# Kernel optimization log

Measured on AMD Instinct MI355X. Metric: run time of the kernel, lower is better.

Reference implementation:

```python
import jax, jax.numpy as jnp
import numpy as np

N = 50000    # nodes
E = 800000   # edges (avg degree 16)
B = 256      # graphs in the batch (static for segment ops)
H = 128      # feature / hidden width (channels[-2])
NL = 4       # LSTM layers in Set2Set
PS = 4       # Set2Set processing steps
OUT = 2      # channels[-1]


def _bn(h, g, b):
    # BatchNorm1d with batch statistics (training-mode math, biased variance)
    m = h.mean(0)
    v = jnp.mean((h - m) ** 2, 0)
    return (h - m) * jax.lax.rsqrt(v + 1e-5) * g + b


def _gin(x, src, dst, W1, b1, ga1, be1, W2, b2, ga2, be2):
    # GINConv, eps=0: out = MLP(x + sum_{j->i} x_j)
    agg = jax.ops.segment_sum(x[src], dst, num_segments=x.shape[0])
    h = x + agg
    h = jax.nn.relu(_bn(h @ W1.T + b1, ga1, be1))
    h = jax.nn.relu(_bn(h @ W2.T + b2, ga2, be2))
    return h


def _set2set(x, batch, Wih0, Whh0, b0, WihR, WhhR, bR):
    hs = [jnp.zeros((B, H), x.dtype)] * NL
    cs = [jnp.zeros((B, H), x.dtype)] * NL
    q_star = jnp.zeros((B, 2 * H), x.dtype)
    for _ in range(PS):
        inp = q_star
        nhs, ncs = [], []
        for l in range(NL):  # stacked LSTM cells, seq-len 1 per step
            Wih = Wih0 if l == 0 else WihR[l - 1]
            Whh = Whh0 if l == 0 else WhhR[l - 1]
            bb = b0 if l == 0 else bR[l - 1]
            gates = inp @ Wih.T + hs[l] @ Whh.T + bb
            i, f, g, o = jnp.split(gates, 4, axis=-1)  # torch gate order i,f,g,o
            c = jax.nn.sigmoid(f) * cs[l] + jax.nn.sigmoid(i) * jnp.tanh(g)
            h = jax.nn.sigmoid(o) * jnp.tanh(c)
            nhs.append(h); ncs.append(c)
            inp = h
        hs, cs = nhs, ncs
        q = inp  # (B, H) top-layer hidden
        # per-graph segment softmax attention
        e = jnp.sum(x * q[batch], -1)                        # (N,)
        m = jax.ops.segment_max(e, batch, num_segments=B)
        ee = jnp.exp(e - m[batch])
        s = jax.ops.segment_sum(ee, batch, num_segments=B)
        a = ee / s[batch]
        r = jax.ops.segment_sum(a[:, None] * x, batch, num_segments=B)  # (B, H)
        q_star = jnp.concatenate([q, r], -1)
    return q_star


def setup_inputs() -> dict:
    key = jax.random.key(0)
    ks = jax.random.split(key, 16)

    def w(k, shape):
        return jax.random.normal(k, shape, jnp.float32) * 0.05

    d = {}
    d["x"] = jax.random.normal(ks[0], (N, H), jnp.float32)
    d["edge_index"] = jax.random.randint(ks[1], (2, E), 0, N, dtype=jnp.int32)
    d["batch"] = jnp.sort(jax.random.randint(ks[2], (N,), 0, B, dtype=jnp.int32))
    for i, g in enumerate(("g0", "g1")):
        kk = jax.random.split(ks[3 + i], 2)
        d[g + "_W1"] = w(kk[0], (H, H)); d[g + "_b1"] = jnp.zeros((H,), jnp.float32)
        d[g + "_gamma1"] = jnp.ones((H,), jnp.float32); d[g + "_beta1"] = jnp.zeros((H,), jnp.float32)
        d[g + "_W2"] = w(kk[1], (H, H)); d[g + "_b2"] = jnp.zeros((H,), jnp.float32)
        d[g + "_gamma2"] = jnp.ones((H,), jnp.float32); d[g + "_beta2"] = jnp.zeros((H,), jnp.float32)
    d["Wih0"] = w(ks[6], (4 * H, 2 * H))
    d["Whh0"] = w(ks[7], (4 * H, H))
    d["b0"] = jnp.zeros((4 * H,), jnp.float32)
    d["WihR"] = w(ks[8], (NL - 1, 4 * H, H))
    d["WhhR"] = w(ks[9], (NL - 1, 4 * H, H))
    d["bR"] = jnp.zeros((NL - 1, 4 * H), jnp.float32)
    d["lin_W"] = w(ks[10], (OUT, 2 * H))
    d["lin_b"] = jnp.zeros((OUT,), jnp.float32)
    return d


def reference(x, edge_index, batch,
              g0_W1, g0_b1, g0_gamma1, g0_beta1, g0_W2, g0_b2, g0_gamma2, g0_beta2,
              g1_W1, g1_b1, g1_gamma1, g1_beta1, g1_W2, g1_b2, g1_gamma2, g1_beta2,
              Wih0, Whh0, b0, WihR, WhhR, bR, lin_W, lin_b):
    src, dst = edge_index[0], edge_index[1]
    x = _gin(x, src, dst, g0_W1, g0_b1, g0_gamma1, g0_beta1, g0_W2, g0_b2, g0_gamma2, g0_beta2)
    x = _gin(x, src, dst, g1_W1, g1_b1, g1_gamma1, g1_beta1, g1_W2, g1_b2, g1_gamma2, g1_beta2)
    q = _set2set(x, batch, Wih0, Whh0, b0, WihR, WhhR, bR)
    # F.dropout(p=0.1) is identity in eval mode
    return q @ lin_W.T + lin_b
```

## Files before the change

kernel.cpp:

```cpp
#include <hip/hip_runtime.h>
#include <math.h>

#define NN 50000
#define EE 800000
#define BBG 256
#define HHC 128
#define SEG_CAP 448
#define ESC 512
#define NBIN 196
#define NBLK 196

typedef _Float16 half8 __attribute__((ext_vector_type(8)));
typedef _Float16 half4 __attribute__((ext_vector_type(4)));
typedef _Float16 half2v __attribute__((ext_vector_type(2)));
typedef float f32x4 __attribute__((ext_vector_type(4)));

#if defined(__has_builtin)
#if __has_builtin(__builtin_amdgcn_fdot2)
#define USE_FDOT2 1
#endif
#endif

__device__ __forceinline__ float fdot2f(half2v a, half2v b, float c) {
#ifdef USE_FDOT2
  return __builtin_amdgcn_fdot2(a, b, c, false);
#else
  return fmaf((float)a[0], (float)b[0], fmaf((float)a[1], (float)b[1], c));
#endif
}

__device__ __forceinline__ float fsigm(float x) {
  return __builtin_amdgcn_rcpf(1.f + __expf(-x));
}
__device__ __forceinline__ float ftanh(float x) {
  return 1.f - 2.f * __builtin_amdgcn_rcpf(1.f + __expf(2.f * x));
}

__device__ __forceinline__ unsigned keyf(float f) {
  unsigned u = __float_as_uint(f);
  return (u & 0x80000000u) ? ~u : (u | 0x80000000u);
}
__device__ __forceinline__ float unkeyf(unsigned k) {
  return (k & 0x80000000u) ? __uint_as_float(k ^ 0x80000000u) : __uint_as_float(~k);
}

__device__ __forceinline__ float4 aff4(float4 v, float4 sc, float4 sh) {
  v.x = fmaxf(fmaf(v.x, sc.x, sh.x), 0.f);
  v.y = fmaxf(fmaf(v.y, sc.y, sh.y), 0.f);
  v.z = fmaxf(fmaf(v.z, sc.z, sh.z), 0.f);
  v.w = fmaxf(fmaf(v.w, sc.w, sh.w), 0.f);
  return v;
}

__global__ __launch_bounds__(256) void prep_all_kernel(
    const int* __restrict__ batch,
    const int* __restrict__ ei,
    const float* __restrict__ W0, const float* __restrict__ W1,
    const float* __restrict__ W2, const float* __restrict__ W3,
    const float* __restrict__ Wih0, const float* __restrict__ Whh0,
    const float* __restrict__ WihR, const float* __restrict__ WhhR,
    const float* __restrict__ b0, const float* __restrict__ bR,
    const float* __restrict__ xsrc,
    float* __restrict__ stats, int* __restrict__ gptr, int* __restrict__ partial,
    _Float16* __restrict__ ginWh, _Float16* __restrict__ WT0h,
    _Float16* __restrict__ WTRh, float* __restrict__ bc0, float* __restrict__ bcR,
    _Float16* __restrict__ x16a) {
  __shared__ int hist[NBIN];
  int blk = blockIdx.x, tid = threadIdx.x;
  if (blk == 0) {
    ((float4*)stats)[tid] = make_float4(0.f, 0.f, 0.f, 0.f);
    return;
  }
  if (blk <= 196) {
    int i = (blk - 1) * 256 + tid;
    if (i >= NN) return;
    int b = batch[i];
    int prev = (i == 0) ? -1 : batch[i - 1];
    for (int g = prev + 1; g <= b; ++g) gptr[g] = i;
    if (i == NN - 1) {
      for (int g = b + 1; g <= BBG; ++g) gptr[g] = NN;
    }
    return;
  }
  if (blk <= 392) {
    int b = blk - 197;
    if (tid < NBIN) hist[tid] = 0;
    __syncthreads();
    const int4* dst4 = (const int4*)(ei + EE);
#pragma unroll
    for (int c = 0; c < 4; ++c) {
      int idx = b * 1024 + c * 256 + tid;
      if (idx < EE / 4) {
        int4 d = dst4[idx];
        atomicAdd(&hist[d.x >> 8], 1);
        atomicAdd(&hist[d.y >> 8], 1);
        atomicAdd(&hist[d.z >> 8], 1);
        atomicAdd(&hist[d.w >> 8], 1);
      }
    }
    __syncthreads();
    if (tid < NBIN) partial[tid * NBLK + b] = hist[tid];
    return;
  }
  if (blk >= 2961) {
    int i = (blk - 2961) * 256 + tid;
    float4 v = ((const float4*)xsrc)[i];
    half4 h;
    h[0] = (_Float16)v.x; h[1] = (_Float16)v.y;
    h[2] = (_Float16)v.z; h[3] = (_Float16)v.w;
    ((half4*)x16a)[i] = h;
    return;
  }
  int idx = (blk - 393) * 256 + tid;
  if (idx < 65536) {
    int m = idx >> 14;
    int r = idx & 16383;
    const float* W = (m == 0) ? W0 : (m == 1) ? W1 : (m == 2) ? W2 : W3;
    ginWh[idx] = (_Float16)W[r];
  } else if (idx < 262144) {
    int t = idx - 65536;
    int k = t >> 9, op = t & 511;
    int j = op >> 2, g = op & 3;
    int row = g * 128 + j;
    float v = (k < 256) ? Wih0[row * 256 + k] : Whh0[row * 128 + (k - 256)];
    WT0h[((k >> 1) << 10) | (op << 1) | (k & 1)] = (_Float16)v;
  } else if (idx < 655360) {
    int t = idx - 262144;
    int l = t >> 17;
    int rem = t & 131071;
    int k = rem >> 9, op = rem & 511;
    int j = op >> 2, g = op & 3;
    int row = g * 128 + j;
    float v = (k < 128) ? WihR[((size_t)l * 512 + row) * 128 + k]
                        : WhhR[((size_t)l * 512 + row) * 128 + (k - 128)];
    WTRh[((size_t)l << 17) | ((k >> 1) << 10) | (op << 1) | (k & 1)] = (_Float16)v;
  } else {
    int t = idx - 655360;
    if (t < 512) {
      bc0[t] = b0[(t & 3) * 128 + (t >> 2)];
    } else {
      int u = t - 512;
      int l = u >> 9, op = u & 511;
      bcR[u] = bR[l * 512 + (op & 3) * 128 + (op >> 2)];
    }
  }
}


__global__ void scan_partials_kernel(const int* __restrict__ partial,
                                     int* __restrict__ block_base, int* __restrict__ total) {
  __shared__ int buf[256];
  int bin = blockIdx.x, tid = threadIdx.x;
  int v = (tid < NBLK) ? partial[bin * NBLK + tid] : 0;
  buf[tid] = v;
  __syncthreads();
  for (int off = 1; off < 256; off <<= 1) {
    int t = (tid >= off) ? buf[tid - off] : 0;
    __syncthreads();
    buf[tid] += t;
    __syncthreads();
  }
  if (tid < NBLK) block_base[bin * NBLK + tid] = buf[tid] - v;
  if (tid == 255) total[bin] = buf[255];
}

__global__ __launch_bounds__(256) void bucket_scatter_kernel(const int* __restrict__ ei,
                                                             const int* __restrict__ total,
                                                             const int* __restrict__ block_base,
                                                             int* __restrict__ packed) {
  __shared__ int sbuf[256];
  __shared__ int cursor[NBIN];
  int tid = threadIdx.x, b = blockIdx.x;
  int v = (tid < NBIN) ? total[tid] : 0;
  sbuf[tid] = v;
  __syncthreads();
  for (int off = 1; off < 256; off <<= 1) {
    int t = (tid >= off) ? sbuf[tid - off] : 0;
    __syncthreads();
    sbuf[tid] += t;
    __syncthreads();
  }
  if (tid < NBIN) cursor[tid] = (sbuf[tid] - v) + block_base[tid * NBLK + b];
  __syncthreads();
  const int4* src4 = (const int4*)ei;
  const int4* dst4 = (const int4*)(ei + EE);
#pragma unroll
  for (int c = 0; c < 4; ++c) {
    int idx = b * 1024 + c * 256 + tid;
    if (idx < EE / 4) {
      int4 s = src4[idx];
      int4 d = dst4[idx];
      int p;
      p = atomicAdd(&cursor[d.x >> 8], 1); packed[p] = (s.x << 8) | (d.x & 255);
      p = atomicAdd(&cursor[d.y >> 8], 1); packed[p] = (s.y << 8) | (d.y & 255);
      p = atomicAdd(&cursor[d.z >> 8], 1); packed[p] = (s.z << 8) | (d.z & 255);
      p = atomicAdd(&cursor[d.w >> 8], 1); packed[p] = (s.w << 8) | (d.w & 255);
    }
  }
}

__global__ __launch_bounds__(256) void csr_finalize_kernel(const int* __restrict__ packed,
                                                           const int* __restrict__ total,
                                                           int* __restrict__ row_start,
                                                           int* __restrict__ csr) {
  __shared__ int fh[256];
  __shared__ int fb[256];
  int bin = blockIdx.x, tid = threadIdx.x;
  int tv = (tid < NBIN) ? total[tid] : 0;
  fb[tid] = tv;
  __syncthreads();
  for (int off = 1; off < 256; off <<= 1) {
    int t = (tid >= off) ? fb[tid - off] : 0;
    __syncthreads();
    fb[tid] += t;
    __syncthreads();
  }
  int e0 = (bin == 0) ? 0 : fb[bin - 1];
  int e1 = fb[bin];
  __syncthreads();
  fh[tid] = 0;
  __syncthreads();
  for (int e = e0 + tid; e < e1; e += 256) atomicAdd(&fh[packed[e] & 255], 1);
  __syncthreads();
  int v = fh[tid];
  fb[tid] = v;
  __syncthreads();
  for (int off = 1; off < 256; off <<= 1) {
    int t = (tid >= off) ? fb[tid - off] : 0;
    __syncthreads();
    fb[tid] += t;
    __syncthreads();
  }
  int excl = fb[tid] - v;
  int node = bin * 256 + tid;
  if (node < NN) row_start[node] = e0 + excl;
  if (bin == NBIN - 1 && tid == 0) row_start[NN] = EE;
  __syncthreads();
  fb[tid] = excl;
  __syncthreads();
  for (int e = e0 + tid; e < e1; e += 256) {
    int p = packed[e];
    int pos = atomicAdd(&fb[p & 255], 1);
    csr[e0 + pos] = p >> 8;
  }
}

template <bool AFF>
__global__ __launch_bounds__(256) void agg_gemm_kernel(
    const _Float16* __restrict__ x16, const int* __restrict__ row_start,
    const int* __restrict__ csr,
    const float* __restrict__ stats, const float* __restrict__ gamma,
    const float* __restrict__ beta,
    const _Float16* __restrict__ Wh, const float* __restrict__ bias,
    _Float16* __restrict__ h16out,
    float* __restrict__ ssum, float* __restrict__ ssq) {
  __shared__ _Float16 As[4][16][136];
  __shared__ float sc_s[128], sh_s[128];
  int tid = threadIdx.x;
  if (AFF) {
    if (tid < 128) {
      const float invN = 1.0f / (float)NN;
      float mm = stats[tid] * invN;
      float vv = stats[128 + tid] * invN - mm * mm;
      float rs = rsqrtf(vv + 1e-5f);
      float sc = gamma[tid] * rs;
      sc_s[tid] = sc;
      sh_s[tid] = beta[tid] - mm * sc;
    }
    __syncthreads();
  }
  int tile0 = blockIdx.x * 4;
  {
    int nloc = tid >> 4;
    int t = tid & 15;
    const half8* xh8 = (const half8*)x16;
    float scv[8], shv[8];
    if (AFF) {
#pragma unroll
      for (int f = 0; f < 8; ++f) { scv[f] = sc_s[t * 8 + f]; shv[f] = sh_s[t * 8 + f]; }
    }
    for (int tt = 0; tt < 4; ++tt) {
      int tile = tile0 + tt;
      if (tile >= 3125) break;
      int node = tile * 16 + nloc;
      int s0 = row_start[node], s1 = row_start[node + 1];
      float acc[8] = {0.f, 0.f, 0.f, 0.f, 0.f, 0.f, 0.f, 0.f};
      int j = s0;
      for (; j + 8 <= s1; j += 8) {
        int i0 = csr[j + 0];
        int i1 = csr[j + 1];
        int i2 = csr[j + 2];
        int i3 = csr[j + 3];
        int i4 = csr[j + 4];
        int i5 = csr[j + 5];
        int i6 = csr[j + 6];
        int i7 = csr[j + 7];
        half8 h0 = xh8[(size_t)i0 * 16 + t];
        half8 h1 = xh8[(size_t)i1 * 16 + t];
        half8 h2 = xh8[(size_t)i2 * 16 + t];
        half8 h3 = xh8[(size_t)i3 * 16 + t];
        half8 h4 = xh8[(size_t)i4 * 16 + t];
        half8 h5 = xh8[(size_t)i5 * 16 + t];
        half8 h6 = xh8[(size_t)i6 * 16 + t];
        half8 h7 = xh8[(size_t)i7 * 16 + t];
#pragma unroll
        for (int f = 0; f < 8; ++f) {
          if (AFF) {
            acc[f] += fmaxf(fmaf((float)h0[f], scv[f], shv[f]), 0.f);
            acc[f] += fmaxf(fmaf((float)h1[f], scv[f], shv[f]), 0.f);
            acc[f] += fmaxf(fmaf((float)h2[f], scv[f], shv[f]), 0.f);
            acc[f] += fmaxf(fmaf((float)h3[f], scv[f], shv[f]), 0.f);
            acc[f] += fmaxf(fmaf((float)h4[f], scv[f], shv[f]), 0.f);
            acc[f] += fmaxf(fmaf((float)h5[f], scv[f], shv[f]), 0.f);
            acc[f] += fmaxf(fmaf((float)h6[f], scv[f], shv[f]), 0.f);
            acc[f] += fmaxf(fmaf((float)h7[f], scv[f], shv[f]), 0.f);
          } else {
            acc[f] += (((float)h0[f] + (float)h1[f]) + ((float)h2[f] + (float)h3[f])) +
                      (((float)h4[f] + (float)h5[f]) + ((float)h6[f] + (float)h7[f]));
          }
        }
      }
      if (j + 4 <= s1) {
        int i0 = csr[j + 0];
        int i1 = csr[j + 1];
        int i2 = csr[j + 2];
        int i3 = csr[j + 3];
        half8 h0 = xh8[(size_t)i0 * 16 + t];
        half8 h1 = xh8[(size_t)i1 * 16 + t];
        half8 h2 = xh8[(size_t)i2 * 16 + t];
        half8 h3 = xh8[(size_t)i3 * 16 + t];
#pragma unroll
        for (int f = 0; f < 8; ++f) {
          if (AFF) {
            acc[f] += fmaxf(fmaf((float)h0[f], scv[f], shv[f]), 0.f);
            acc[f] += fmaxf(fmaf((float)h1[f], scv[f], shv[f]), 0.f);
            acc[f] += fmaxf(fmaf((float)h2[f], scv[f], shv[f]), 0.f);
            acc[f] += fmaxf(fmaf((float)h3[f], scv[f], shv[f]), 0.f);
          } else {
            acc[f] += ((float)h0[f] + (float)h1[f]) + ((float)h2[f] + (float)h3[f]);
          }
        }
        j += 4;
      }
      for (; j < s1; ++j) {
        int i = csr[j];
        half8 h = xh8[(size_t)i * 16 + t];
#pragma unroll
        for (int f = 0; f < 8; ++f) {
          float v = (float)h[f];
          if (AFF) v = fmaxf(fmaf(v, scv[f], shv[f]), 0.f);
          acc[f] += v;
        }
      }
      half8 selfh = xh8[(size_t)node * 16 + t];
      half8 hv;
#pragma unroll
      for (int f = 0; f < 8; ++f) {
        float sv = (float)selfh[f];
        if (AFF) sv = fmaxf(fmaf(sv, scv[f], shv[f]), 0.f);
        hv[f] = (_Float16)(acc[f] + sv);
      }
      *(half8*)&As[tt][nloc][t * 8] = hv;
    }
  }
  __syncthreads();
  int w = tid >> 6, l = tid & 63;
  int lr = l & 15, lg = l >> 4;
  int cb = w * 32;
  half8 bf0[4], bf1[4];
#pragma unroll
  for (int ks = 0; ks < 4; ++ks) {
    int k = ks * 32 + lg * 8;
    bf0[ks] = *(const half8*)(Wh + (size_t)(cb + lr) * 128 + k);
    bf1[ks] = *(const half8*)(Wh + (size_t)(cb + 16 + lr) * 128 + k);
  }
  float bv0 = bias[cb + lr], bv1 = bias[cb + 16 + lr];
  float ps0 = 0.f, pq0 = 0.f, ps1 = 0.f, pq1 = 0.f;
  for (int tt = 0; tt < 4; ++tt) {
    int tile = tile0 + tt;
    if (tile >= 3125) break;
    half8 af[4];
#pragma unroll
    for (int ks = 0; ks < 4; ++ks) {
      af[ks] = *(const half8*)&As[tt][lr][ks * 32 + lg * 8];
    }
    f32x4 acc0 = {0.f, 0.f, 0.f, 0.f};
    f32x4 acc1 = {0.f, 0.f, 0.f, 0.f};
#pragma unroll
    for (int ks = 0; ks < 4; ++ks) {
      acc0 = __builtin_amdgcn_mfma_f32_16x16x32_f16(af[ks], bf0[ks], acc0, 0, 0, 0);
      acc1 = __builtin_amdgcn_mfma_f32_16x16x32_f16(af[ks], bf1[ks], acc1, 0, 0, 0);
    }
#pragma unroll
    for (int i = 0; i < 4; ++i) {
      int rr = tile * 16 + lg * 4 + i;
      float v0 = acc0[i] + bv0;
      float v1 = acc1[i] + bv1;
      h16out[(size_t)rr * 128 + cb + lr] = (_Float16)v0;
      h16out[(size_t)rr * 128 + cb + 16 + lr] = (_Float16)v1;
      ps0 += v0; pq0 += v0 * v0;
      ps1 += v1; pq1 += v1 * v1;
    }
  }
  ps0 += __shfl_xor(ps0, 16); ps0 += __shfl_xor(ps0, 32);
  pq0 += __shfl_xor(pq0, 16); pq0 += __shfl_xor(pq0, 32);
  ps1 += __shfl_xor(ps1, 16); ps1 += __shfl_xor(ps1, 32);
  pq1 += __shfl_xor(pq1, 16); pq1 += __shfl_xor(pq1, 32);
  if (lg == 0) {
    atomicAdd(&ssum[cb + lr], ps0);
    atomicAdd(&ssq[cb + lr], pq0);
    atomicAdd(&ssum[cb + 16 + lr], ps1);
    atomicAdd(&ssq[cb + 16 + lr], pq1);
  }
}

template <bool BN>
__global__ __launch_bounds__(256) void gemm_gin_mfma_kernel(
    const _Float16* __restrict__ A16,
    const _Float16* __restrict__ Wh,
    const float* __restrict__ bias,
    const float* __restrict__ stats, const float* __restrict__ gamma,
    const float* __restrict__ beta,
    _Float16* __restrict__ h16out,
    float* __restrict__ ssum, float* __restrict__ ssq) {
  __shared__ float bsc_s[128], bsh_s[128];
  int tid = threadIdx.x;
  if (BN) {
    if (tid < 128) {
      const float invN = 1.0f / (float)NN;
      float mm = stats[tid] * invN;
      float vv = stats[128 + tid] * invN - mm * mm;
      float rs = rsqrtf(vv + 1e-5f);
      float sc = gamma[tid] * rs;
      bsc_s[tid] = sc;
      bsh_s[tid] = beta[tid] - mm * sc;
    }
    __syncthreads();
  }
  int w = tid >> 6, l = tid & 63;
  int lr = l & 15, lg = l >> 4;
  int cb = w * 32;
  half8 bf0[4], bf1[4];
#pragma unroll
  for (int ks = 0; ks < 4; ++ks) {
    int k = ks * 32 + lg * 8;
    bf0[ks] = *(const half8*)(Wh + (size_t)(cb + lr) * 128 + k);
    bf1[ks] = *(const half8*)(Wh + (size_t)(cb + 16 + lr) * 128 + k);
  }
  float bv0 = bias[cb + lr], bv1 = bias[cb + 16 + lr];
  float ps0 = 0.f, pq0 = 0.f, ps1 = 0.f, pq1 = 0.f;
  int t0 = blockIdx.x * 4;
  for (int t = 0; t < 4; ++t) {
    int tile = t0 + t;
    if (tile >= 3125) break;
    int r = tile * 16 + lr;
    half8 af[4];
#pragma unroll
    for (int ks = 0; ks < 4; ++ks) {
      int k0 = ks * 32 + lg * 8;
      half8 ah = *(const half8*)(A16 + (size_t)r * 128 + k0);
      if constexpr (BN) {
        float4 s0 = *(const float4*)&bsc_s[k0];
        float4 s1 = *(const float4*)&bsc_s[k0 + 4];
        float4 h0 = *(const float4*)&bsh_s[k0];
        float4 h1 = *(const float4*)&bsh_s[k0 + 4];
        half8 o;
        o[0] = (_Float16)fmaxf(fmaf((float)ah[0], s0.x, h0.x), 0.f);
        o[1] = (_Float16)fmaxf(fmaf((float)ah[1], s0.y, h0.y), 0.f);
        o[2] = (_Float16)fmaxf(fmaf((float)ah[2], s0.z, h0.z), 0.f);
        o[3] = (_Float16)fmaxf(fmaf((float)ah[3], s0.w, h0.w), 0.f);
        o[4] = (_Float16)fmaxf(fmaf((float)ah[4], s1.x, h1.x), 0.f);
        o[5] = (_Float16)fmaxf(fmaf((float)ah[5], s1.y, h1.y), 0.f);
        o[6] = (_Float16)fmaxf(fmaf((float)ah[6], s1.z, h1.z), 0.f);
        o[7] = (_Float16)fmaxf(fmaf((float)ah[7], s1.w, h1.w), 0.f);
        af[ks] = o;
      } else {
        af[ks] = ah;
      }
    }
    f32x4 acc0 = {0.f, 0.f, 0.f, 0.f};
    f32x4 acc1 = {0.f, 0.f, 0.f, 0.f};
#pragma unroll
    for (int ks = 0; ks < 4; ++ks) {
      acc0 = __builtin_amdgcn_mfma_f32_16x16x32_f16(af[ks], bf0[ks], acc0, 0, 0, 0);
      acc1 = __builtin_amdgcn_mfma_f32_16x16x32_f16(af[ks], bf1[ks], acc1, 0, 0, 0);
    }
#pragma unroll
    for (int i = 0; i < 4; ++i) {
      int rr = tile * 16 + lg * 4 + i;
      float v0 = acc0[i] + bv0;
      float v1 = acc1[i] + bv1;
      h16out[(size_t)rr * 128 + cb + lr] = (_Float16)v0;
      h16out[(size_t)rr * 128 + cb + 16 + lr] = (_Float16)v1;
      ps0 += v0; pq0 += v0 * v0;
      ps1 += v1; pq1 += v1 * v1;
    }
  }
  ps0 += __shfl_xor(ps0, 16); ps0 += __shfl_xor(ps0, 32);
  pq0 += __shfl_xor(pq0, 16); pq0 += __shfl_xor(pq0, 32);
  ps1 += __shfl_xor(ps1, 16); ps1 += __shfl_xor(ps1, 32);
  pq1 += __shfl_xor(pq1, 16); pq1 += __shfl_xor(pq1, 32);
  if (lg == 0) {
    atomicAdd(&ssum[cb + lr], ps0);
    atomicAdd(&ssq[cb + lr], pq0);
    atomicAdd(&ssum[cb + 16 + lr], ps1);
    atomicAdd(&ssq[cb + 16 + lr], pq1);
  }
}

__global__ void __launch_bounds__(1024) set2set_kernel(
    const _Float16* __restrict__ x, const int* __restrict__ gptr,
    const float* __restrict__ stats, const float* __restrict__ gamma,
    const float* __restrict__ beta,
    const _Float16* __restrict__ WT0h, const _Float16* __restrict__ WTRh,
    const float* __restrict__ bc0, const float* __restrict__ bcR,
    float* __restrict__ ebuf,
    const float* __restrict__ linW, const float* __restrict__ linb,
    float* __restrict__ out) {
  __shared__ half2v xs[SEG_CAP * 64];
  __shared__ float wpart[16][512];
  __shared__ float hcs[4][128];
  __shared__ float ccs[4][128];
  __shared__ _Float16 h16s[4][128];
  __shared__ _Float16 q16s[256];
  __shared__ float qst[256];
  __shared__ float es[ESC];
  __shared__ float bsc[128], bsh[128];
  __shared__ unsigned smax_u;
  __shared__ float ssum_s;
  __shared__ float fred[2][4];

  int g = blockIdx.x, tid = threadIdx.x;
  int w16 = tid >> 6, lane = tid & 63;

  if (tid < 128) {
    const float invN = 1.0f / (float)NN;
    float mm = stats[tid] * invN;
    float vv = stats[128 + tid] * invN - mm * mm;
    float rs = rsqrtf(vv + 1e-5f);
    float sc = gamma[tid] * rs;
    bsc[tid] = sc;
    bsh[tid] = beta[tid] - mm * sc;
#pragma unroll
    for (int l = 0; l < 4; ++l) {
      hcs[l][tid] = 0.f; ccs[l][tid] = 0.f; h16s[l][tid] = (_Float16)0.f;
    }
  }
  if (tid < 256) { qst[tid] = 0.f; q16s[tid] = (_Float16)0.f; }
  __syncthreads();

  int s0 = gptr[g], s1 = gptr[g + 1];
  int seg = s1 - s0;
  int ncache = seg < SEG_CAP ? seg : SEG_CAP;
  const half2v* xh = (const half2v*)x;
  float sc0 = bsc[2 * lane], sc1 = bsc[2 * lane + 1];
  float sh0 = bsh[2 * lane], sh1 = bsh[2 * lane + 1];
  for (int n = w16; n < ncache; n += 16) {
    half2v v = xh[(size_t)(s0 + n) * 64 + lane];
    half2v h;
    h[0] = (_Float16)fmaxf(fmaf((float)v[0], sc0, sh0), 0.f);
    h[1] = (_Float16)fmaxf(fmaf((float)v[1], sc1, sh1), 0.f);
    xs[n * 64 + lane] = h;
  }
  __syncthreads();

  int s_ = tid >> 6, cg = tid & 63;

  for (int step = 0; step < 4; ++step) {
    for (int cell = 0; cell < 4; ++cell) {
      const _Float16* WTh; const float* bias; int KP2;
      if (cell == 0) {
        WTh = WT0h; bias = bc0; KP2 = 12;
      } else {
        WTh = WTRh + (size_t)(cell - 1) * 131072;
        bias = bcR + (cell - 1) * 512; KP2 = 8;
      }
      bool skipmv = (step == 0 && cell == 0);
      if (!skipmv) {
        int se = (s_ + g) & 15;
        int k20 = se * KP2;
        float a0 = 0.f, a1 = 0.f, a2 = 0.f, a3 = 0.f;
        float a4 = 0.f, a5 = 0.f, a6 = 0.f, a7 = 0.f;
        if (step != 0 || se < 8) {
          const char* wb = (const char*)WTh + (size_t)k20 * 2048 + (cg << 5);
#pragma unroll 4
          for (int k2 = 0; k2 < KP2; ++k2) {
            uint4 wa = *(const uint4*)(wb + (size_t)k2 * 2048);
            uint4 wc = *(const uint4*)(wb + (size_t)k2 * 2048 + 16);
            int kk = (k20 + k2) << 1;
            half2v i2;
            if (cell == 0) {
              i2 = (kk < 256) ? *(const half2v*)&q16s[kk]
                              : *(const half2v*)&h16s[0][kk - 256];
            } else {
              i2 = (kk < 128) ? *(const half2v*)&h16s[cell - 1][kk]
                              : *(const half2v*)&h16s[cell][kk - 128];
            }
            a0 = fdot2f(i2, __builtin_bit_cast(half2v, wa.x), a0);
            a1 = fdot2f(i2, __builtin_bit_cast(half2v, wa.y), a1);
            a2 = fdot2f(i2, __builtin_bit_cast(half2v, wa.z), a2);
            a3 = fdot2f(i2, __builtin_bit_cast(half2v, wa.w), a3);
            a4 = fdot2f(i2, __builtin_bit_cast(half2v, wc.x), a4);
            a5 = fdot2f(i2, __builtin_bit_cast(half2v, wc.y), a5);
            a6 = fdot2f(i2, __builtin_bit_cast(half2v, wc.z), a6);
            a7 = fdot2f(i2, __builtin_bit_cast(half2v, wc.w), a7);
          }
        }
        *(float4*)&wpart[s_][cg << 3] = make_float4(a0, a1, a2, a3);
        *(float4*)(&wpart[s_][cg << 3] + 4) = make_float4(a4, a5, a6, a7);
        __syncthreads();
      }
      if (tid < 128) {
        int j = tid;
        float4 ga = *(const float4*)&bias[4 * j];
        if (!skipmv) {
#pragma unroll
          for (int s = 0; s < 16; ++s) {
            float4 wv = *(const float4*)&wpart[s][4 * j];
            ga.x += wv.x; ga.y += wv.y; ga.z += wv.z; ga.w += wv.w;
          }
        }
        float cp = ccs[cell][j];
        float si = fsigm(ga.x);
        float sf = fsigm(ga.y);
        float so = fsigm(ga.w);
        float cn = sf * cp + si * ftanh(ga.z);
        ccs[cell][j] = cn;
        float hn = so * ftanh(cn);
        hcs[cell][j] = hn;
        h16s[cell][j] = (_Float16)hn;
        if (cell == 3 && j == 0) { smax_u = 0u; ssum_s = 0.f; }
      }
      __syncthreads();
    }
    float* rpart = &wpart[0][0];
    float qx = hcs[3][2 * lane], qy = hcs[3][2 * lane + 1];
    half2v q2; q2[0] = (_Float16)qx; q2[1] = (_Float16)qy;
    float wmax = -3.0e38f;
    for (int n = w16; n < seg; n += 16) {
      float e;
      if (n < ncache) {
        e = fdot2f(xs[n * 64 + lane], q2, 0.f);
      } else {
        half2v v = xh[(size_t)(s0 + n) * 64 + lane];
        float vx = fmaxf(fmaf((float)v[0], sc0, sh0), 0.f);
        float vy = fmaxf(fmaf((float)v[1], sc1, sh1), 0.f);
        e = vx * qx + vy * qy;
      }
#pragma unroll
      for (int sh = 32; sh; sh >>= 1) e += __shfl_xor(e, sh);
      if (lane == 0) { if (n < ESC) es[n] = e; else ebuf[s0 + n] = e; }
      wmax = fmaxf(wmax, e);
    }
    if (lane == 0) atomicMax(&smax_u, keyf(wmax));
    __syncthreads();
    float m = unkeyf(smax_u);
    float loc = 0.f;
    for (int n = tid; n < seg; n += 1024) {
      float e = (n < ESC) ? es[n] : ebuf[s0 + n];
      float ex = __expf(e - m);
      if (n < ESC) es[n] = ex; else ebuf[s0 + n] = ex;
      loc += ex;
    }
#pragma unroll
    for (int sh = 32; sh; sh >>= 1) loc += __shfl_xor(loc, sh);
    if (lane == 0) atomicAdd(&ssum_s, loc);
    __syncthreads();
    float inv = 1.0f / ssum_s;
    float rx = 0.f, ry = 0.f;
    for (int n = w16; n < seg; n += 16) {
      float ex = (n < ESC) ? es[n] : ebuf[s0 + n];
      float coef = ex * inv;
      float vx, vy;
      if (n < ncache) {
        half2v v2 = xs[n * 64 + lane];
        vx = (float)v2[0]; vy = (float)v2[1];
      } else {
        half2v v = xh[(size_t)(s0 + n) * 64 + lane];
        vx = fmaxf(fmaf((float)v[0], sc0, sh0), 0.f);
        vy = fmaxf(fmaf((float)v[1], sc1, sh1), 0.f);
      }
      rx += coef * vx; ry += coef * vy;
    }
    rpart[w16 * 128 + 2 * lane] = rx;
    rpart[w16 * 128 + 2 * lane + 1] = ry;
    __syncthreads();
    if (tid < 128) {
      float r = 0.f;
#pragma unroll
      for (int t = 0; t < 16; ++t) r += rpart[t * 128 + tid];
      float h3 = hcs[3][tid];
      qst[tid] = h3;
      qst[128 + tid] = r;
      q16s[tid] = (_Float16)h3;
      q16s[128 + tid] = (_Float16)r;
    }
    __syncthreads();
  }
  if (tid < 256) {
    float val = qst[tid];
    float p0 = val * linW[tid];
    float p1 = val * linW[256 + tid];
#pragma unroll
    for (int sh = 32; sh; sh >>= 1) { p0 += __shfl_xor(p0, sh); p1 += __shfl_xor(p1, sh); }
    if (lane == 0) { fred[0][w16] = p0; fred[1][w16] = p1; }
  }
  __syncthreads();
  if (tid == 0) {
    out[2 * g + 0] = fred[0][0] + fred[0][1] + fred[0][2] + fred[0][3] + linb[0];
    out[2 * g + 1] = fred[1][0] + fred[1][1] + fred[1][2] + fred[1][3] + linb[1];
  }
}


extern "C" void kernel_launch(void* const* d_in, const int* in_sizes, int n_in,
                              void* d_out, int out_size, void* d_ws, size_t ws_size,
                              hipStream_t stream) {
  const float* x = (const float*)d_in[0];
  const int* ei = (const int*)d_in[1];
  const int* batch = (const int*)d_in[2];
  const float* gW[4]  = {(const float*)d_in[3],  (const float*)d_in[7],
                         (const float*)d_in[11], (const float*)d_in[15]};
  const float* gb[4]  = {(const float*)d_in[4],  (const float*)d_in[8],
                         (const float*)d_in[12], (const float*)d_in[16]};
  const float* gga[4] = {(const float*)d_in[5],  (const float*)d_in[9],
                         (const float*)d_in[13], (const float*)d_in[17]};
  const float* gbe[4] = {(const float*)d_in[6],  (const float*)d_in[10],
                         (const float*)d_in[14], (const float*)d_in[18]};
  const float* Wih0 = (const float*)d_in[19];
  const float* Whh0 = (const float*)d_in[20];
  const float* b0   = (const float*)d_in[21];
  const float* WihR = (const float*)d_in[22];
  const float* WhhR = (const float*)d_in[23];
  const float* bR   = (const float*)d_in[24];
  const float* linW = (const float*)d_in[25];
  const float* linb = (const float*)d_in[26];
  float* out = (float*)d_out;

  char* base = (char*)d_ws;
  size_t off = 0;
  auto allocf = [&](size_t n) { float* p = (float*)(base + off); off += n * sizeof(float); return p; };
  _Float16* bufA = (_Float16*)(base + off); off += 6400000 * 2;
  _Float16* bufB = (_Float16*)(base + off); off += 6400000 * 2;
  _Float16* bufC = (_Float16*)(base + off); off += 6400000 * 2;
  _Float16* ginWh = (_Float16*)(base + off); off += 65536 * 2;
  _Float16* WT0h = (_Float16*)(base + off); off += 196608 * 2;
  _Float16* WTRh = (_Float16*)(base + off); off += 393216 * 2;
  float* bc0   = allocf(512);
  float* bcR   = allocf(1536);
  float* ebuf  = allocf(50000);
  float* stats = allocf(1024);
  int* row_start = (int*)(base + off); off += 50004 * 4;
  int* gptr = (int*)(base + off); off += 260 * 4;
  int* csr = (int*)(base + off); off += 800000 * 4;
  int* packed = (int*)(base + off); off += 800000 * 4;
  int* partial = (int*)(base + off); off += NBIN * NBLK * 4;
  int* block_base = (int*)(base + off); off += NBIN * NBLK * 4;
  int* total = (int*)(base + off); off += 256 * 4;
  (void)ws_size; (void)in_sizes; (void)n_in; (void)out_size;

  prep_all_kernel<<<9211, 256, 0, stream>>>(batch, ei, gW[0], gW[1], gW[2], gW[3],
                                            Wih0, Whh0, WihR, WhhR, b0, bR, x,
                                            stats, gptr, partial, ginWh, WT0h, WTRh,
                                            bc0, bcR, bufA);
  scan_partials_kernel<<<NBIN, 256, 0, stream>>>(partial, block_base, total);
  bucket_scatter_kernel<<<NBLK, 256, 0, stream>>>(ei, total, block_base, packed);
  csr_finalize_kernel<<<NBIN, 256, 0, stream>>>(packed, total, row_start, csr);

  agg_gemm_kernel<false><<<782, 256, 0, stream>>>(
      bufA, row_start, csr,
      nullptr, nullptr, nullptr,
      ginWh + 0 * 16384, gb[0],
      bufB, stats + 0, stats + 128);
  gemm_gin_mfma_kernel<true><<<782, 256, 0, stream>>>(
      bufB, ginWh + 1 * 16384, gb[1],
      stats + 0, gga[0], gbe[0],
      bufC, stats + 256, stats + 384);
  agg_gemm_kernel<true><<<782, 256, 0, stream>>>(
      bufC, row_start, csr,
      stats + 256, gga[1], gbe[1],
      ginWh + 2 * 16384, gb[2],
      bufB, stats + 512, stats + 640);
  gemm_gin_mfma_kernel<true><<<782, 256, 0, stream>>>(
      bufB, ginWh + 3 * 16384, gb[3],
      stats + 512, gga[2], gbe[2],
      bufA, stats + 768, stats + 896);

  set2set_kernel<<<256, 1024, 0, stream>>>(bufA, gptr, stats + 768, gga[3], gbe[3],
                                           WT0h, WTRh, bc0, bcR, ebuf, linW, linb, out);
}
```

Before: 406.1 us.

## Process two graphs per set2set block to share LSTM weight loads

The set2set kernel now handles two graphs per 1024-thread block (128 blocks instead of 256). Each weight vector loaded for the LSTM mat-vec is applied to both graphs' inputs, which halves weight traffic per graph. The attention phase splits the block into two groups of 8 waves, one per graph. In exchange, the per-graph node cache shrinks from 448 to 144 rows, so larger graphs fall back to global reads more often. Only 128 blocks are launched, so parallelism drops on a 256-CU device.

```diff
diff --git a/kernel.cpp b/kernel.cpp
--- a/kernel.cpp
+++ b/kernel.cpp
@@ -5,8 +5,8 @@
 #define EE 800000
 #define BBG 256
 #define HHC 128
-#define SEG_CAP 448
-#define ESC 512
+#define SEG2 144
+#define ESC2 256
 #define NBIN 196
 #define NBLK 196
 
@@ -517,21 +517,24 @@
     float* __restrict__ ebuf,
     const float* __restrict__ linW, const float* __restrict__ linb,
     float* __restrict__ out) {
-  __shared__ half2v xs[SEG_CAP * 64];
-  __shared__ float wpart[16][512];
-  __shared__ float hcs[4][128];
-  __shared__ float ccs[4][128];
-  __shared__ _Float16 h16s[4][128];
-  __shared__ _Float16 q16s[256];
-  __shared__ float qst[256];
-  __shared__ float es[ESC];
+  __shared__ half2v xs[2][SEG2][64];
+  __shared__ float wpart[2][16][512];
+  __shared__ float hcs[2][4][128];
+  __shared__ float ccs[2][4][128];
+  __shared__ _Float16 h16s[2][4][128];
+  __shared__ _Float16 q16s[2][256];
+  __shared__ float qst[2][256];
+  __shared__ float es[2][ESC2];
   __shared__ float bsc[128], bsh[128];
-  __shared__ unsigned smax_u;
-  __shared__ float ssum_s;
-  __shared__ float fred[2][4];
-
-  int g = blockIdx.x, tid = threadIdx.x;
+  __shared__ unsigned smax_u[2];
+  __shared__ float ssum_s[2];
+  __shared__ float fred[2][2][4];
+
+  int gA = blockIdx.x * 2;
+  int tid = threadIdx.x;
   int w16 = tid >> 6, lane = tid & 63;
+  int s_ = w16, cg = lane;
+  int grs = w16 >> 3, wl = w16 & 7;
 
   if (tid < 128) {
     const float invN = 1.0f / (float)NN;
@@ -541,46 +544,48 @@
     float sc = gamma[tid] * rs;
     bsc[tid] = sc;
     bsh[tid] = beta[tid] - mm * sc;
+  }
+  if (tid < 256) {
+    int gr = tid >> 7, j = tid & 127;
 #pragma unroll
     for (int l = 0; l < 4; ++l) {
-      hcs[l][tid] = 0.f; ccs[l][tid] = 0.f; h16s[l][tid] = (_Float16)0.f;
-    }
-  }
-  if (tid < 256) { qst[tid] = 0.f; q16s[tid] = (_Float16)0.f; }
-  __syncthreads();
-
-  int s0 = gptr[g], s1 = gptr[g + 1];
-  int seg = s1 - s0;
-  int ncache = seg < SEG_CAP ? seg : SEG_CAP;
+      hcs[gr][l][j] = 0.f; ccs[gr][l][j] = 0.f; h16s[gr][l][j] = (_Float16)0.f;
+    }
+  }
+  if (tid < 512) {
+    int gr = tid >> 8, idx = tid & 255;
+    qst[gr][idx] = 0.f; q16s[gr][idx] = (_Float16)0.f;
+  }
+  __syncthreads();
+
+  int sg0 = gptr[gA + grs], sgend = gptr[gA + grs + 1];
+  int segg = sgend - sg0;
+  int ncg = segg < SEG2 ? segg : SEG2;
   const half2v* xh = (const half2v*)x;
   float sc0 = bsc[2 * lane], sc1 = bsc[2 * lane + 1];
   float sh0 = bsh[2 * lane], sh1 = bsh[2 * lane + 1];
-  for (int n = w16; n < ncache; n += 16) {
-    half2v v = xh[(size_t)(s0 + n) * 64 + lane];
+  for (int n = wl; n < ncg; n += 8) {
+    half2v v = xh[(size_t)(sg0 + n) * 64 + lane];
     half2v h;
     h[0] = (_Float16)fmaxf(fmaf((float)v[0], sc0, sh0), 0.f);
     h[1] = (_Float16)fmaxf(fmaf((float)v[1], sc1, sh1), 0.f);
-    xs[n * 64 + lane] = h;
-  }
-  __syncthreads();
-
-  int s_ = tid >> 6, cg = tid & 63;
+    xs[grs][n][lane] = h;
+  }
+  __syncthreads();
 
   for (int step = 0; step < 4; ++step) {
     for (int cell = 0; cell < 4; ++cell) {
       const _Float16* WTh; const float* bias; int KP2;
-      if (cell == 0) {
-        WTh = WT0h; bias = bc0; KP2 = 12;
-      } else {
-        WTh = WTRh + (size_t)(cell - 1) * 131072;
-        bias = bcR + (cell - 1) * 512; KP2 = 8;
-      }
+      if (cell == 0) { WTh = WT0h; bias = bc0; KP2 = 12; }
+      else { WTh = WTRh + (size_t)(cell - 1) * 131072; bias = bcR + (cell - 1) * 512; KP2 = 8; }
       bool skipmv = (step == 0 && cell == 0);
       if (!skipmv) {
-        int se = (s_ + g) & 15;
+        int se = (s_ + gA) & 15;
         int k20 = se * KP2;
         float a0 = 0.f, a1 = 0.f, a2 = 0.f, a3 = 0.f;
         float a4 = 0.f, a5 = 0.f, a6 = 0.f, a7 = 0.f;
+        float b0 = 0.f, b1 = 0.f, b2 = 0.f, b3 = 0.f;
+        float b4 = 0.f, b5 = 0.f, b6 = 0.f, b7 = 0.f;
         if (step != 0 || se < 8) {
           const char* wb = (const char*)WTh + (size_t)k20 * 2048 + (cg << 5);
 #pragma unroll 4
@@ -588,127 +593,156 @@
             uint4 wa = *(const uint4*)(wb + (size_t)k2 * 2048);
             uint4 wc = *(const uint4*)(wb + (size_t)k2 * 2048 + 16);
             int kk = (k20 + k2) << 1;
-            half2v i2;
+            half2v iA, iB;
             if (cell == 0) {
-              i2 = (kk < 256) ? *(const half2v*)&q16s[kk]
-                              : *(const half2v*)&h16s[0][kk - 256];
+              iA = (kk < 256) ? *(const half2v*)&q16s[0][kk]
+                              : *(const half2v*)&h16s[0][0][kk - 256];
+              iB = (kk < 256) ? *(const half2v*)&q16s[1][kk]
+                              : *(const half2v*)&h16s[1][0][kk - 256];
             } else {
-              i2 = (kk < 128) ? *(const half2v*)&h16s[cell - 1][kk]
-                              : *(const half2v*)&h16s[cell][kk - 128];
+              iA = (kk < 128) ? *(const half2v*)&h16s[0][cell - 1][kk]
+                              : *(const half2v*)&h16s[0][cell][kk - 128];
+              iB = (kk < 128) ? *(const half2v*)&h16s[1][cell - 1][kk]
+                              : *(const half2v*)&h16s[1][cell][kk - 128];
             }
-            a0 = fdot2f(i2, __builtin_bit_cast(half2v, wa.x), a0);
-            a1 = fdot2f(i2, __builtin_bit_cast(half2v, wa.y), a1);
-            a2 = fdot2f(i2, __builtin_bit_cast(half2v, wa.z), a2);
-            a3 = fdot2f(i2, __builtin_bit_cast(half2v, wa.w), a3);
-            a4 = fdot2f(i2, __builtin_bit_cast(half2v, wc.x), a4);
-            a5 = fdot2f(i2, __builtin_bit_cast(half2v, wc.y), a5);
-            a6 = fdot2f(i2, __builtin_bit_cast(half2v, wc.z), a6);
-            a7 = fdot2f(i2, __builtin_bit_cast(half2v, wc.w), a7);
+            half2v v0 = __builtin_bit_cast(half2v, wa.x);
+            half2v v1 = __builtin_bit_cast(half2v, wa.y);
+            half2v v2 = __builtin_bit_cast(half2v, wa.z);
+            half2v v3 = __builtin_bit_cast(half2v, wa.w);
+            half2v v4 = __builtin_bit_cast(half2v, wc.x);
+            half2v v5 = __builtin_bit_cast(half2v, wc.y);
+            half2v v6 = __builtin_bit_cast(half2v, wc.z);
+            half2v v7 = __builtin_bit_cast(half2v, wc.w);
+            a0 = fdot2f(iA, v0, a0); b0 = fdot2f(iB, v0, b0);
+            a1 = fdot2f(iA, v1, a1); b1 = fdot2f(iB, v1, b1);
+            a2 = fdot2f(iA, v2, a2); b2 = fdot2f(iB, v2, b2);
+            a3 = fdot2f(iA, v3, a3); b3 = fdot2f(iB, v3, b3);
+            a4 = fdot2f(iA, v4, a4); b4 = fdot2f(iB, v4, b4);
+            a5 = fdot2f(iA, v5, a5); b5 = fdot2f(iB, v5, b5);
+            a6 = fdot2f(iA, v6, a6); b6 = fdot2f(iB, v6, b6);
+            a7 = fdot2f(iA, v7, a7); b7 = fdot2f(iB, v7, b7);
           }
         }
-        *(float4*)&wpart[s_][cg << 3] = make_float4(a0, a1, a2, a3);
-        *(float4*)(&wpart[s_][cg << 3] + 4) = make_float4(a4, a5, a6, a7);
+        *(float4*)&wpart[0][s_][cg << 3] = make_float4(a0, a1, a2, a3);
+        *(float4*)(&wpart[0][s_][cg << 3] + 4) = make_float4(a4, a5, a6, a7);
+        *(float4*)&wpart[1][s_][cg << 3] = make_float4(b0, b1, b2, b3);
+        *(float4*)(&wpart[1][s_][cg << 3] + 4) = make_float4(b4, b5, b6, b7);
         __syncthreads();
       }
-      if (tid < 128) {
-        int j = tid;
+      if (tid < 256) {
+        int gr = tid >> 7, j = tid & 127;
         float4 ga = *(const float4*)&bias[4 * j];
         if (!skipmv) {
 #pragma unroll
           for (int s = 0; s < 16; ++s) {
-            float4 wv = *(const float4*)&wpart[s][4 * j];
+            float4 wv = *(const float4*)&wpart[gr][s][4 * j];
             ga.x += wv.x; ga.y += wv.y; ga.z += wv.z; ga.w += wv.w;
           }
         }
-        float cp = ccs[cell][j];
+        float cp = ccs[gr][cell][j];
         float si = fsigm(ga.x);
         float sf = fsigm(ga.y);
         float so = fsigm(ga.w);
         float cn = sf * cp + si * ftanh(ga.z);
-        ccs[cell][j] = cn;
+        ccs[gr][cell][j] = cn;
         float hn = so * ftanh(cn);
-        hcs[cell][j] = hn;
-        h16s[cell][j] = (_Float16)hn;
-        if (cell == 3 && j == 0) { smax_u = 0u; ssum_s = 0.f; }
+        hcs[gr][cell][j] = hn;
+        h16s[gr][cell][j] = (_Float16)hn;
+        if (cell == 3 && j == 0) { smax_u[gr] = 0u; ssum_s[gr] = 0.f; }
       }
       __syncthreads();
     }
-    float* rpart = &wpart[0][0];
-    float qx = hcs[3][2 * lane], qy = hcs[3][2 * lane + 1];
+    float qx = hcs[grs][3][2 * lane], qy = hcs[grs][3][2 * lane + 1];
     half2v q2; q2[0] = (_Float16)qx; q2[1] = (_Float16)qy;
     float wmax = -3.0e38f;
-    for (int n = w16; n < seg; n += 16) {
+    for (int n = wl; n < segg; n += 8) {
       float e;
-      if (n < ncache) {
-        e = fdot2f(xs[n * 64 + lane], q2, 0.f);
+      if (n < ncg) {
+        e = fdot2f(xs[grs][n][lane], q2, 0.f);
       } else {
-        half2v v = xh[(size_t)(s0 + n) * 64 + lane];
+        half2v v = xh[(size_t)(sg0 + n) * 64 + lane];
         float vx = fmaxf(fmaf((float)v[0], sc0, sh0), 0.f);
         float vy = fmaxf(fmaf((float)v[1], sc1, sh1), 0.f);
         e = vx * qx + vy * qy;
       }
 #pragma unroll
       for (int sh = 32; sh; sh >>= 1) e += __shfl_xor(e, sh);
-      if (lane == 0) { if (n < ESC) es[n] = e; else ebuf[s0 + n] = e; }
+      if (lane == 0) { if (n < ESC2) es[grs][n] = e; else ebuf[sg0 + n] = e; }
       wmax = fmaxf(wmax, e);
     }
-    if (lane == 0) atomicMax(&smax_u, keyf(wmax));
-    __syncthreads();
-    float m = unkeyf(smax_u);
-    float loc = 0.f;
-    for (int n = tid; n < seg; n += 1024) {
-      float e = (n < ESC) ? es[n] : ebuf[s0 + n];
-      float ex = __expf(e - m);
-      if (n < ESC) es[n] = ex; else ebuf[s0 + n] = ex;
-      loc += ex;
-    }
-#pragma unroll
-    for (int sh = 32; sh; sh >>= 1) loc += __shfl_xor(loc, sh);
-    if (lane == 0) atomicAdd(&ssum_s, loc);
-    __syncthreads();
-    float inv = 1.0f / ssum_s;
+    if (lane == 0) atomicMax(&smax_u[grs], keyf(wmax));
+    __syncthreads();
+    {
+      int gr2 = tid >> 9;
+      int p0g = gptr[gA + gr2];
+      int segp = gptr[gA + gr2 + 1] - p0g;
+      float m2 = unkeyf(smax_u[gr2]);
+      float loc = 0.f;
+      for (int n = tid & 511; n < segp; n += 512) {
+        float e = (n < ESC2) ? es[gr2][n] : ebuf[p0g + n];
+        float ex = __expf(e - m2);
+        if (n < ESC2) es[gr2][n] = ex; else ebuf[p0g + n] = ex;
+        loc += ex;
+      }
+#pragma unroll
+      for (int sh = 32; sh; sh >>= 1) loc += __shfl_xor(loc, sh);
+      if (lane == 0) atomicAdd(&ssum_s[gr2], loc);
+    }
+    __syncthreads();
+    float inv = 1.0f / ssum_s[grs];
+    float* rp = &wpart[grs][0][0];
     float rx = 0.f, ry = 0.f;
-    for (int n = w16; n < seg; n += 16) {
-      float ex = (n < ESC) ? es[n] : ebuf[s0 + n];
+    for (int n = wl; n < segg; n += 8) {
+      float ex = (n < ESC2) ? es[grs][n] : ebuf[sg0 + n];
       float coef = ex * inv;
       float vx, vy;
-      if (n < ncache) {
-        half2v v2 = xs[n * 64 + lane];
+      if (n < ncg) {
+        half2v v2 = xs[grs][n][lane];
         vx = (float)v2[0]; vy = (float)v2[1];
       } else {
-        half2v v = xh[(size_t)(s0 + n) * 64 + lane];
+        half2v v = xh[(size_t)(sg0 + n) * 64 + lane];
         vx = fmaxf(fmaf((float)v[0], sc0, sh0), 0.f);
         vy = fmaxf(fmaf((float)v[1], sc1, sh1), 0.f);
       }
       rx += coef * vx; ry += coef * vy;
     }
-    rpart[w16 * 128 + 2 * lane] = rx;
-    rpart[w16 * 128 + 2 * lane + 1] = ry;
-    __syncthreads();
-    if (tid < 128) {
+    rp[wl * 128 + 2 * lane] = rx;
+    rp[wl * 128 + 2 * lane + 1] = ry;
+    __syncthreads();
+    if (tid < 256) {
+      int gr = tid >> 7, j = tid & 127;
+      const float* rpg = &wpart[gr][0][0];
       float r = 0.f;
 #pragma unroll
-      for (int t = 0; t < 16; ++t) r += rpart[t * 128 + tid];
-      float h3 = hcs[3][tid];
-      qst[tid] = h3;
-      qst[128 + tid] = r;
-      q16s[tid] = (_Float16)h3;
-      q16s[128 + tid] = (_Float16)r;
-    }
-    __syncthreads();
-  }
-  if (tid < 256) {
-    float val = qst[tid];
-    float p0 = val * linW[tid];
-    float p1 = val * linW[256 + tid];
+      for (int t = 0; t < 8; ++t) r += rpg[t * 128 + j];
+      float h3 = hcs[gr][3][j];
+      qst[gr][j] = h3;
+      qst[gr][128 + j] = r;
+      q16s[gr][j] = (_Float16)h3;
+      q16s[gr][128 + j] = (_Float16)r;
+    }
+    __syncthreads();
+  }
+  if (tid < 512) {
+    int gr = tid >> 8, idx = tid & 255;
+    float val = qst[gr][idx];
+    float p0 = val * linW[idx];
+    float p1 = val * linW[256 + idx];
 #pragma unroll
     for (int sh = 32; sh; sh >>= 1) { p0 += __shfl_xor(p0, sh); p1 += __shfl_xor(p1, sh); }
-    if (lane == 0) { fred[0][w16] = p0; fred[1][w16] = p1; }
+    if (lane == 0) {
+      int ws = (tid >> 6) & 3;
+      fred[gr][0][ws] = p0; fred[gr][1][ws] = p1;
+    }
   }
   __syncthreads();
   if (tid == 0) {
-    out[2 * g + 0] = fred[0][0] + fred[0][1] + fred[0][2] + fred[0][3] + linb[0];
-    out[2 * g + 1] = fred[1][0] + fred[1][1] + fred[1][2] + fred[1][3] + linb[1];
+    out[2 * gA + 0] = fred[0][0][0] + fred[0][0][1] + fred[0][0][2] + fred[0][0][3] + linb[0];
+    out[2 * gA + 1] = fred[0][1][0] + fred[0][1][1] + fred[0][1][2] + fred[0][1][3] + linb[1];
+  }
+  if (tid == 64) {
+    out[2 * gA + 2] = fred[1][0][0] + fred[1][0][1] + fred[1][0][2] + fred[1][0][3] + linb[0];
+    out[2 * gA + 3] = fred[1][1][0] + fred[1][1][1] + fred[1][1][2] + fred[1][1][3] + linb[1];
   }
 }
 
@@ -786,6 +820,6 @@
       stats + 512, gga[2], gbe[2],
       bufA, stats + 768, stats + 896);
 
-  set2set_kernel<<<256, 1024, 0, stream>>>(bufA, gptr, stats + 768, gga[3], gbe[3],
+  set2set_kernel<<<128, 1024, 0, stream>>>(bufA, gptr, stats + 768, gga[3], gbe[3],
                                            WT0h, WTRh, bc0, bcR, ebuf, linW, linb, out);
 }
```

After: 440.8 us. 1.09x slower.
